# Performance work log

Hardware: AMD Instinct MI355X
Metric: run time of the kernel (lower is better)

The kernel has to match this reference:

```python
import math
import jax, jax.numpy as jnp
import numpy as np

H, DK = 16, 64            # n_heads, d_kv
NUM_BUCKETS, MAX_DIST = 32, 128


def _relative_position_buckets(S):
    # Bidirectional (encoder) T5 bucketization of relative positions.
    ctx = jnp.arange(S, dtype=jnp.int32)[:, None]      # query positions
    mem = jnp.arange(S, dtype=jnp.int32)[None, :]      # key positions
    rp = mem - ctx                                     # [S, S]
    nb = NUM_BUCKETS // 2
    rb = (rp > 0).astype(jnp.int32) * nb
    n = jnp.abs(rp)
    max_exact = nb // 2
    is_small = n < max_exact
    large = max_exact + (
        jnp.log(jnp.maximum(n, 1).astype(jnp.float32) / max_exact)
        / math.log(MAX_DIST / max_exact)
        * (nb - max_exact)
    ).astype(jnp.int32)
    large = jnp.minimum(large, nb - 1)
    return rb + jnp.where(is_small, n, large)          # [S, S] int32


def setup_inputs() -> dict:
    key = jax.random.key(0)
    ks = jax.random.split(key, 6)
    B, S, D = 4, 1024, 1024
    inner = H * DK
    std = 0.02
    return {
        "hidden_states": jax.random.normal(ks[0], (B, S, D), jnp.float32),
        "Wq": jax.random.normal(ks[1], (inner, D), jnp.float32) * std,
        "Wk": jax.random.normal(ks[2], (inner, D), jnp.float32) * std,
        "Wv": jax.random.normal(ks[3], (inner, D), jnp.float32) * std,
        "Wo": jax.random.normal(ks[4], (D, inner), jnp.float32) * std,
        "rel_bias": jax.random.normal(ks[5], (NUM_BUCKETS, H), jnp.float32) * std,
    }


def reference(hidden_states, Wq, Wk, Wv, Wo, rel_bias):
    B, S, D = hidden_states.shape

    def proj(W):  # bias-free linear + split heads -> [B, H, S, DK]
        return (hidden_states @ W.T).reshape(B, S, H, DK).transpose(0, 2, 1, 3)

    q, k, v = proj(Wq), proj(Wk), proj(Wv)
    # T5: NO 1/sqrt(d) scaling
    scores = jnp.einsum("bhqd,bhkd->bhqk", q, k)       # [B, H, S, S]
    bias = rel_bias[_relative_position_buckets(S)]     # [S, S, H]
    scores = scores + bias.transpose(2, 0, 1)[None]    # broadcast over batch
    attn = jax.nn.softmax(scores, axis=-1)
    ctx = jnp.einsum("bhqk,bhkd->bhqd", attn, v)       # [B, H, S, DK]
    ctx = ctx.transpose(0, 2, 1, 3).reshape(B, S, H * DK)
    return ctx @ Wo.T                                  # [B, S, D]
```

## Files before the change

### kernel.cpp

```cpp
#include <hip/hip_runtime.h>

typedef _Float16 half8 __attribute__((ext_vector_type(8)));
typedef _Float16 half4_t __attribute__((ext_vector_type(4)));
typedef float f32x4 __attribute__((ext_vector_type(4)));

#define GK 1024
#define MEG (1024 * 1024)
#define LOG2E 1.44269504088896f

#define GLD16(gptr, lptr) \
    __builtin_amdgcn_global_load_lds((const __attribute__((address_space(1))) void*)(gptr), \
                                     (__attribute__((address_space(3))) void*)(lptr), 16, 0, 0)

__global__ void cvt_all_kernel(const float* __restrict__ hidden,
                               const float* __restrict__ Wq,
                               const float* __restrict__ Wk,
                               const float* __restrict__ Wv,
                               const float* __restrict__ Wo,
                               _Float16* __restrict__ ws) {
    int b = blockIdx.x;
    const float* src;
    _Float16* dst;
    if (b < 4096)      { src = hidden; dst = ws; }
    else if (b < 5120) { src = Wq; dst = ws + 4 * MEG; b -= 4096; }
    else if (b < 6144) { src = Wk; dst = ws + 5 * MEG; b -= 5120; }
    else if (b < 7168) { src = Wv; dst = ws + 6 * MEG; b -= 6144; }
    else               { src = Wo; dst = ws + 7 * MEG; b -= 7168; }
    int i = (b * 256 + threadIdx.x) * 4;
    f32x4 v = *(const f32x4*)(src + i);
    half4_t h;
    h[0] = (_Float16)v[0]; h[1] = (_Float16)v[1];
    h[2] = (_Float16)v[2]; h[3] = (_Float16)v[3];
    *(half4_t*)(dst + i) = h;
}

__global__ __launch_bounds__(256) void gemm_qkv_kernel(
    const _Float16* __restrict__ A,
    const _Float16* __restrict__ B0,
    const _Float16* __restrict__ B1,
    const _Float16* __restrict__ B2,
    _Float16* __restrict__ O0,
    _Float16* __restrict__ O1,
    _Float16* __restrict__ O2)
{
    const int lid = blockIdx.x;
    const int xcd = lid & 7;
    const int rr = lid >> 3;
    const int xb = rr & 7;
    const int gg = xcd * 12 + (rr >> 3);
    const int yb = gg & 31;
    const int z  = gg >> 5;
    const _Float16* Bw = (z == 0) ? B0 : ((z == 1) ? B1 : B2);
    _Float16* Oh = (z == 0) ? O0 : ((z == 1) ? O1 : O2);

    __shared__ __attribute__((aligned(16))) _Float16 sA[2][128][32];
    __shared__ __attribute__((aligned(16))) _Float16 sB[2][128][32];

    const int tid = threadIdx.x;
    const int wave = tid >> 6, lane = tid & 63;
    const int quad = lane >> 4, l16 = lane & 15;
    const int wr = wave >> 1, wc = wave & 1;
    const int M0 = yb * 128, N0 = xb * 128;

    const int rl = lane >> 2;
    const int cl = (lane & 3) * 8;
    const size_t aRow0 = (size_t)(M0 + wave * 16 + rl) * GK + cl;
    const size_t aRow1 = aRow0 + (size_t)64 * GK;
    const size_t bRow0 = (size_t)(N0 + wave * 16 + rl) * GK + cl;
    const size_t bRow1 = bRow0 + (size_t)64 * GK;
    _Float16* ldsA[2][2] = {{&sA[0][wave * 16][0], &sA[0][64 + wave * 16][0]},
                            {&sA[1][wave * 16][0], &sA[1][64 + wave * 16][0]}};
    _Float16* ldsB[2][2] = {{&sB[0][wave * 16][0], &sB[0][64 + wave * 16][0]},
                            {&sB[1][wave * 16][0], &sB[1][64 + wave * 16][0]}};

    f32x4 acc[4][4] = {};

    for (int kt = 0; kt < GK / 64; ++kt) {
        const int ko = kt * 64;
        #pragma unroll
        for (int c = 0; c < 2; ++c) {
            GLD16(A + aRow0 + ko + c * 32, ldsA[c][0]);
            GLD16(A + aRow1 + ko + c * 32, ldsA[c][1]);
            GLD16(Bw + bRow0 + ko + c * 32, ldsB[c][0]);
            GLD16(Bw + bRow1 + ko + c * 32, ldsB[c][1]);
        }
        __syncthreads();
        #pragma unroll
        for (int c = 0; c < 2; ++c) {
            half8 af[4], bf[4];
            #pragma unroll
            for (int i = 0; i < 4; ++i)
                af[i] = *(const half8*)&sA[c][wr * 64 + i * 16 + l16][quad * 8];
            #pragma unroll
            for (int j = 0; j < 4; ++j)
                bf[j] = *(const half8*)&sB[c][wc * 64 + j * 16 + l16][quad * 8];
            #pragma unroll
            for (int i = 0; i < 4; ++i)
                #pragma unroll
                for (int j = 0; j < 4; ++j)
                    acc[i][j] = __builtin_amdgcn_mfma_f32_16x16x32_f16(af[i], bf[j], acc[i][j], 0, 0, 0);
        }
        __syncthreads();
    }

    if (z == 2) {
        #pragma unroll
        for (int i = 0; i < 4; ++i) {
            #pragma unroll
            for (int j = 0; j < 4; ++j) {
                int m = M0 + wr * 64 + i * 16 + quad * 4;
                int n = N0 + wc * 64 + j * 16 + l16;
                int b = m >> 10, s = m & 1023, hh = n >> 6, d = n & 63;
                half4_t o;
                #pragma unroll
                for (int r = 0; r < 4; ++r) o[r] = (_Float16)acc[i][j][r];
                *(half4_t*)&Oh[((size_t)((b * 16 + hh) * 64 + d)) * 1024 + s] = o;
            }
        }
    } else {
        #pragma unroll
        for (int i = 0; i < 4; ++i) {
            #pragma unroll
            for (int j = 0; j < 4; ++j) {
                #pragma unroll
                for (int r = 0; r < 4; ++r) {
                    int m = M0 + wr * 64 + i * 16 + quad * 4 + r;
                    int n = N0 + wc * 64 + j * 16 + l16;
                    int b = m >> 10, s = m & 1023, hh = n >> 6, d = n & 63;
                    Oh[((size_t)((b * 16 + hh) * 1024 + s)) * 64 + d] = (_Float16)acc[i][j][r];
                }
            }
        }
    }
}

__global__ __launch_bounds__(256) void gemm_o_kernel(
    const _Float16* __restrict__ A,
    const _Float16* __restrict__ Bw,
    float* __restrict__ Of)
{
    const int lid = blockIdx.x;
    const int xcd = lid & 7;
    const int rr = lid >> 3;
    const int xb = rr & 7;
    const int yb = xcd * 8 + (rr >> 3);

    __shared__ __attribute__((aligned(16))) _Float16 sA[2][64][32];
    __shared__ __attribute__((aligned(16))) _Float16 sB[2][128][32];

    const int tid = threadIdx.x;
    const int wave = tid >> 6, lane = tid & 63;
    const int quad = lane >> 4, l16 = lane & 15;
    const int M0 = yb * 64, N0 = xb * 128;

    const int rl = lane >> 2;
    const int cl = (lane & 3) * 8;
    const size_t aRow  = (size_t)(M0 + wave * 16 + rl) * GK + cl;
    const size_t bRow0 = (size_t)(N0 + wave * 16 + rl) * GK + cl;
    const size_t bRow1 = bRow0 + (size_t)64 * GK;
    _Float16* ldsA[2]    = {&sA[0][wave * 16][0], &sA[1][wave * 16][0]};
    _Float16* ldsB[2][2] = {{&sB[0][wave * 16][0], &sB[0][64 + wave * 16][0]},
                            {&sB[1][wave * 16][0], &sB[1][64 + wave * 16][0]}};

    f32x4 acc[4][2] = {};

    for (int kt = 0; kt < GK / 64; ++kt) {
        const int ko = kt * 64;
        #pragma unroll
        for (int c = 0; c < 2; ++c) {
            GLD16(A + aRow + ko + c * 32, ldsA[c]);
            GLD16(Bw + bRow0 + ko + c * 32, ldsB[c][0]);
            GLD16(Bw + bRow1 + ko + c * 32, ldsB[c][1]);
        }
        __syncthreads();
        #pragma unroll
        for (int c = 0; c < 2; ++c) {
            half8 af[4], bf[2];
            #pragma unroll
            for (int i = 0; i < 4; ++i)
                af[i] = *(const half8*)&sA[c][i * 16 + l16][quad * 8];
            #pragma unroll
            for (int j = 0; j < 2; ++j)
                bf[j] = *(const half8*)&sB[c][wave * 32 + j * 16 + l16][quad * 8];
            #pragma unroll
            for (int i = 0; i < 4; ++i)
                #pragma unroll
                for (int j = 0; j < 2; ++j)
                    acc[i][j] = __builtin_amdgcn_mfma_f32_16x16x32_f16(af[i], bf[j], acc[i][j], 0, 0, 0);
        }
        __syncthreads();
    }

    #pragma unroll
    for (int i = 0; i < 4; ++i) {
        #pragma unroll
        for (int j = 0; j < 2; ++j) {
            #pragma unroll
            for (int r = 0; r < 4; ++r) {
                int m = M0 + i * 16 + quad * 4 + r;
                int n = N0 + wave * 32 + j * 16 + l16;
                Of[(size_t)m * 1024 + n] = acc[i][j][r];
            }
        }
    }
}

__global__ __launch_bounds__(256) void attn_kernel(
    const _Float16* __restrict__ Q,
    const _Float16* __restrict__ K,
    const _Float16* __restrict__ VT,
    const float* __restrict__ rel_bias,
    _Float16* __restrict__ ctx)
{
    const int S = 1024;
    const int qt = blockIdx.x;
    const int q0 = qt * 64;
    const int h = blockIdx.y;
    const int b = blockIdx.z;
    const int bh = b * 16 + h;
    const _Float16* Qh = Q + (size_t)bh * S * 64;
    const _Float16* Kh = K + (size_t)bh * S * 64;
    const _Float16* VTh = VT + (size_t)bh * 64 * S;

    __shared__ __attribute__((aligned(16))) _Float16 sQ[64][72];
    __shared__ __attribute__((aligned(16))) _Float16 sK[64][72];
    __shared__ __attribute__((aligned(16))) _Float16 sVt[64][72];
    __shared__ __attribute__((aligned(16))) _Float16 sP[4][16][72];
    __shared__ _Float16 sBias[1088];

    const int tid = threadIdx.x;
    const int wave = tid >> 6, lane = tid & 63;
    const int quad = lane >> 4, l16 = lane & 15;

    {
        int r = tid >> 3, c = (tid & 7) * 8;
        *(half8*)&sQ[r][c]      = *(const half8*)(Qh + (size_t)(q0 + r) * 64 + c);
        *(half8*)&sQ[r + 32][c] = *(const half8*)(Qh + (size_t)(q0 + r + 32) * 64 + c);
    }
    for (int i = tid; i < 1087; i += 256) {
        int delta = i - (q0 + 63);
        int rb = (delta > 0) ? 16 : 0;
        int n = (delta < 0) ? -delta : delta;
        int bucket;
        if (n < 8) bucket = rb + n;
        else bucket = rb + 8 + (n >= 12) + (n >= 16) + (n >= 23) + (n >= 32)
                             + (n >= 46) + (n >= 64) + (n >= 91);
        sBias[i] = (_Float16)rel_bias[bucket * 16 + h];
    }
    __syncthreads();

    half8 qf0 = *(const half8*)&sQ[wave * 16 + l16][quad * 8];
    half8 qf1 = *(const half8*)&sQ[wave * 16 + l16][32 + quad * 8];

    const int sr = tid >> 3;
    const int sc_ = (tid & 7) * 8;
    const _Float16* kp0 = Kh + (size_t)sr * 64 + sc_;
    const _Float16* kp1 = kp0 + (size_t)32 * 64;
    const _Float16* vp0 = VTh + (size_t)sr * S + sc_;
    const _Float16* vp1 = vp0 + (size_t)32 * S;
    _Float16* sKw0 = &sK[sr][sc_];
    _Float16* sKw1 = &sK[sr + 32][sc_];
    _Float16* sVw0 = &sVt[sr][sc_];
    _Float16* sVw1 = &sVt[sr + 32][sc_];

    half8 rk0 = *(const half8*)kp0;
    half8 rk1 = *(const half8*)kp1;
    half8 rv0 = *(const half8*)vp0;
    half8 rv1 = *(const half8*)vp1;
    kp0 += 4096; kp1 += 4096; vp0 += 64; vp1 += 64;

    float m_run = -INFINITY, l_run = 0.0f;
    f32x4 acc[4] = {};

    for (int kt = 0; kt < 16; ++kt) {
        __syncthreads();
        *(half8*)sKw0 = rk0;
        *(half8*)sKw1 = rk1;
        *(half8*)sVw0 = rv0;
        *(half8*)sVw1 = rv1;
        __syncthreads();
        if (kt < 15) {
            rk0 = *(const half8*)kp0;
            rk1 = *(const half8*)kp1;
            rv0 = *(const half8*)vp0;
            rv1 = *(const half8*)vp1;
            kp0 += 4096; kp1 += 4096; vp0 += 64; vp1 += 64;
        }

        f32x4 sc[4] = {};
        #pragma unroll
        for (int j = 0; j < 4; ++j) {
            half8 kf0 = *(const half8*)&sK[j * 16 + l16][quad * 8];
            half8 kf1 = *(const half8*)&sK[j * 16 + l16][32 + quad * 8];
            sc[j] = __builtin_amdgcn_mfma_f32_16x16x32_f16(kf0, qf0, sc[j], 0, 0, 0);
            sc[j] = __builtin_amdgcn_mfma_f32_16x16x32_f16(kf1, qf1, sc[j], 0, 0, 0);
        }

        const int bbase = kt * 64 + quad * 4 - wave * 16 - l16 + 63;
        float ps = 0.0f;
        if (kt <= qt - 3 || kt >= qt + 3) {
            const float cb = (float)sBias[bbase];
            float mx = fmaxf(fmaxf(fmaxf(sc[0][0], sc[0][1]), fmaxf(sc[0][2], sc[0][3])),
                             fmaxf(fmaxf(sc[1][0], sc[1][1]), fmaxf(sc[1][2], sc[1][3])));
            mx = fmaxf(mx, fmaxf(fmaxf(fmaxf(sc[2][0], sc[2][1]), fmaxf(sc[2][2], sc[2][3])),
                                 fmaxf(fmaxf(sc[3][0], sc[3][1]), fmaxf(sc[3][2], sc[3][3]))));
            mx = fmaxf(mx, __shfl_xor(mx, 16));
            mx = fmaxf(mx, __shfl_xor(mx, 32));
            float mnew = fmaxf(m_run, mx + cb);
            float alpha = __expf(m_run - mnew);
            m_run = mnew;
            const float kk = (cb - mnew) * LOG2E;
            #pragma unroll
            for (int j = 0; j < 4; ++j) {
                half4_t pw;
                #pragma unroll
                for (int r = 0; r < 4; ++r) {
                    float p = __builtin_exp2f(__builtin_fmaf(sc[j][r], LOG2E, kk));
                    ps += p;
                    pw[r] = (_Float16)p;
                }
                *(half4_t*)&sP[wave][l16][j * 16 + quad * 4] = pw;
            }
            l_run = l_run * alpha + ps;
            #pragma unroll
            for (int dt = 0; dt < 4; ++dt) acc[dt] *= alpha;
        } else {
            #pragma unroll
            for (int j = 0; j < 4; ++j)
                #pragma unroll
                for (int r = 0; r < 4; ++r)
                    sc[j][r] += (float)sBias[bbase + j * 16 + r];
            float mx = fmaxf(fmaxf(fmaxf(sc[0][0], sc[0][1]), fmaxf(sc[0][2], sc[0][3])),
                             fmaxf(fmaxf(sc[1][0], sc[1][1]), fmaxf(sc[1][2], sc[1][3])));
            mx = fmaxf(mx, fmaxf(fmaxf(fmaxf(sc[2][0], sc[2][1]), fmaxf(sc[2][2], sc[2][3])),
                                 fmaxf(fmaxf(sc[3][0], sc[3][1]), fmaxf(sc[3][2], sc[3][3]))));
            mx = fmaxf(mx, __shfl_xor(mx, 16));
            mx = fmaxf(mx, __shfl_xor(mx, 32));
            float mnew = fmaxf(m_run, mx);
            float alpha = __expf(m_run - mnew);
            m_run = mnew;
            #pragma unroll
            for (int j = 0; j < 4; ++j) {
                half4_t pw;
                #pragma unroll
                for (int r = 0; r < 4; ++r) {
                    float p = __expf(sc[j][r] - mnew);
                    ps += p;
                    pw[r] = (_Float16)p;
                }
                *(half4_t*)&sP[wave][l16][j * 16 + quad * 4] = pw;
            }
            l_run = l_run * alpha + ps;
            #pragma unroll
            for (int dt = 0; dt < 4; ++dt) acc[dt] *= alpha;
        }

        half8 pf0 = *(const half8*)&sP[wave][l16][quad * 8];
        half8 pf1 = *(const half8*)&sP[wave][l16][32 + quad * 8];
        #pragma unroll
        for (int dt = 0; dt < 4; ++dt) {
            half8 vf0 = *(const half8*)&sVt[dt * 16 + l16][quad * 8];
            half8 vf1 = *(const half8*)&sVt[dt * 16 + l16][32 + quad * 8];
            acc[dt] = __builtin_amdgcn_mfma_f32_16x16x32_f16(vf0, pf0, acc[dt], 0, 0, 0);
            acc[dt] = __builtin_amdgcn_mfma_f32_16x16x32_f16(vf1, pf1, acc[dt], 0, 0, 0);
        }
    }

    l_run += __shfl_xor(l_run, 16);
    l_run += __shfl_xor(l_run, 32);
    const float inv = 1.0f / l_run;
    const size_t qg = (size_t)(b * 1024 + q0 + wave * 16 + l16);
    #pragma unroll
    for (int dt = 0; dt < 4; ++dt) {
        half4_t o;
        #pragma unroll
        for (int r = 0; r < 4; ++r) o[r] = (_Float16)(acc[dt][r] * inv);
        *(half4_t*)&ctx[qg * 1024 + h * 64 + dt * 16 + quad * 4] = o;
    }
}

extern "C" void kernel_launch(void* const* d_in, const int* in_sizes, int n_in,
                              void* d_out, int out_size, void* d_ws, size_t ws_size,
                              hipStream_t stream) {
    const float* hidden   = (const float*)d_in[0];
    const float* Wq       = (const float*)d_in[1];
    const float* Wk       = (const float*)d_in[2];
    const float* Wv       = (const float*)d_in[3];
    const float* Wo       = (const float*)d_in[4];
    const float* rel_bias = (const float*)d_in[5];
    float* out = (float*)d_out;

    _Float16* ws    = (_Float16*)d_ws;
    _Float16* h16   = ws;
    _Float16* wq16  = ws + 4 * (size_t)MEG;
    _Float16* wk16  = ws + 5 * (size_t)MEG;
    _Float16* wv16  = ws + 6 * (size_t)MEG;
    _Float16* wo16  = ws + 7 * (size_t)MEG;
    _Float16* Qs    = ws + 8 * (size_t)MEG;
    _Float16* Ks    = ws + 12 * (size_t)MEG;
    _Float16* VTs   = ws + 16 * (size_t)MEG;
    _Float16* ctx16 = ws + 20 * (size_t)MEG;

    cvt_all_kernel<<<8192, 256, 0, stream>>>(hidden, Wq, Wk, Wv, Wo, ws);

    gemm_qkv_kernel<<<dim3(768), 256, 0, stream>>>(
        h16, wq16, wk16, wv16, Qs, Ks, VTs);

    attn_kernel<<<dim3(16, 16, 4), 256, 0, stream>>>(Qs, Ks, VTs, rel_bias, ctx16);

    gemm_o_kernel<<<dim3(512), 256, 0, stream>>>(ctx16, wo16, out);
}
```

Measured before the change: 191.6 us.

## Enlarge attention tiles to 128x128 with 512 threads and remap QKV GEMM blocks

The attention kernel now processes 128 queries per block with 8 waves and steps through keys in 128-wide tiles, so each block loads K and V half as many times. The two softmax branches are merged into one path with a uniform-bias flag, and P·V is done in two 64-key halves that reuse the same per-wave P buffer. The QKV GEMM block index mapping is changed so each XCD handles four fixed row blocks across all three weights, aiming for better L2 reuse of the activation matrix. The costs are fewer blocks in the attention launch and higher register and LDS use per block, which could reduce occupancy.

Measured after the change: 200.3 us. +4.5%, slower.

```diff
diff --git a/kernel.cpp b/kernel.cpp
--- a/kernel.cpp
+++ b/kernel.cpp
@@ -47,9 +47,9 @@
     const int xcd = lid & 7;
     const int rr = lid >> 3;
     const int xb = rr & 7;
-    const int gg = xcd * 12 + (rr >> 3);
-    const int yb = gg & 31;
-    const int z  = gg >> 5;
+    const int gidx = rr >> 3;
+    const int yb = xcd * 4 + (gidx & 3);
+    const int z  = gidx >> 2;
     const _Float16* Bw = (z == 0) ? B0 : ((z == 1) ? B1 : B2);
     _Float16* Oh = (z == 0) ? O0 : ((z == 1) ? O1 : O2);
 
@@ -205,7 +205,7 @@
     }
 }
 
-__global__ __launch_bounds__(256) void attn_kernel(
+__global__ __launch_bounds__(512) void attn_kernel(
     const _Float16* __restrict__ Q,
     const _Float16* __restrict__ K,
     const _Float16* __restrict__ VT,
@@ -214,7 +214,7 @@
 {
     const int S = 1024;
     const int qt = blockIdx.x;
-    const int q0 = qt * 64;
+    const int q0 = qt * 128;
     const int h = blockIdx.y;
     const int b = blockIdx.z;
     const int bh = b * 16 + h;
@@ -222,11 +222,11 @@
     const _Float16* Kh = K + (size_t)bh * S * 64;
     const _Float16* VTh = VT + (size_t)bh * 64 * S;
 
-    __shared__ __attribute__((aligned(16))) _Float16 sQ[64][72];
-    __shared__ __attribute__((aligned(16))) _Float16 sK[64][72];
-    __shared__ __attribute__((aligned(16))) _Float16 sVt[64][72];
-    __shared__ __attribute__((aligned(16))) _Float16 sP[4][16][72];
-    __shared__ _Float16 sBias[1088];
+    __shared__ __attribute__((aligned(16))) _Float16 sQ[128][72];
+    __shared__ __attribute__((aligned(16))) _Float16 sK[128][72];
+    __shared__ __attribute__((aligned(16))) _Float16 sVt[64][136];
+    __shared__ __attribute__((aligned(16))) _Float16 sP[8][16][72];
+    __shared__ _Float16 sBias[1152];
 
     const int tid = threadIdx.x;
     const int wave = tid >> 6, lane = tid & 63;
@@ -235,10 +235,10 @@
     {
         int r = tid >> 3, c = (tid & 7) * 8;
         *(half8*)&sQ[r][c]      = *(const half8*)(Qh + (size_t)(q0 + r) * 64 + c);
-        *(half8*)&sQ[r + 32][c] = *(const half8*)(Qh + (size_t)(q0 + r + 32) * 64 + c);
-    }
-    for (int i = tid; i < 1087; i += 256) {
-        int delta = i - (q0 + 63);
+        *(half8*)&sQ[r + 64][c] = *(const half8*)(Qh + (size_t)(q0 + r + 64) * 64 + c);
+    }
+    for (int i = tid; i < 1151; i += 512) {
+        int delta = i - (q0 + 127);
         int rb = (delta > 0) ? 16 : 0;
         int n = (delta < 0) ? -delta : delta;
         int bucket;
@@ -255,115 +255,126 @@
     const int sr = tid >> 3;
     const int sc_ = (tid & 7) * 8;
     const _Float16* kp0 = Kh + (size_t)sr * 64 + sc_;
-    const _Float16* kp1 = kp0 + (size_t)32 * 64;
-    const _Float16* vp0 = VTh + (size_t)sr * S + sc_;
+    const _Float16* kp1 = kp0 + (size_t)64 * 64;
+    _Float16* sKw0 = &sK[sr][sc_];
+    _Float16* sKw1 = &sK[sr + 64][sc_];
+    const int vr = tid >> 4;
+    const int vc = (tid & 15) * 8;
+    const _Float16* vp0 = VTh + (size_t)vr * S + vc;
     const _Float16* vp1 = vp0 + (size_t)32 * S;
-    _Float16* sKw0 = &sK[sr][sc_];
-    _Float16* sKw1 = &sK[sr + 32][sc_];
-    _Float16* sVw0 = &sVt[sr][sc_];
-    _Float16* sVw1 = &sVt[sr + 32][sc_];
+    _Float16* sVw0 = &sVt[vr][vc];
+    _Float16* sVw1 = &sVt[vr + 32][vc];
 
     half8 rk0 = *(const half8*)kp0;
     half8 rk1 = *(const half8*)kp1;
     half8 rv0 = *(const half8*)vp0;
     half8 rv1 = *(const half8*)vp1;
-    kp0 += 4096; kp1 += 4096; vp0 += 64; vp1 += 64;
+    kp0 += 8192; kp1 += 8192; vp0 += 128; vp1 += 128;
 
     float m_run = -INFINITY, l_run = 0.0f;
     f32x4 acc[4] = {};
 
-    for (int kt = 0; kt < 16; ++kt) {
+    for (int kt = 0; kt < 8; ++kt) {
         __syncthreads();
         *(half8*)sKw0 = rk0;
         *(half8*)sKw1 = rk1;
         *(half8*)sVw0 = rv0;
         *(half8*)sVw1 = rv1;
         __syncthreads();
-        if (kt < 15) {
+        if (kt < 7) {
             rk0 = *(const half8*)kp0;
             rk1 = *(const half8*)kp1;
             rv0 = *(const half8*)vp0;
             rv1 = *(const half8*)vp1;
-            kp0 += 4096; kp1 += 4096; vp0 += 64; vp1 += 64;
-        }
-
-        f32x4 sc[4] = {};
-        #pragma unroll
-        for (int j = 0; j < 4; ++j) {
+            kp0 += 8192; kp1 += 8192; vp0 += 128; vp1 += 128;
+        }
+
+        f32x4 sc[8] = {};
+        #pragma unroll
+        for (int j = 0; j < 8; ++j) {
             half8 kf0 = *(const half8*)&sK[j * 16 + l16][quad * 8];
             half8 kf1 = *(const half8*)&sK[j * 16 + l16][32 + quad * 8];
             sc[j] = __builtin_amdgcn_mfma_f32_16x16x32_f16(kf0, qf0, sc[j], 0, 0, 0);
             sc[j] = __builtin_amdgcn_mfma_f32_16x16x32_f16(kf1, qf1, sc[j], 0, 0, 0);
         }
 
-        const int bbase = kt * 64 + quad * 4 - wave * 16 - l16 + 63;
-        float ps = 0.0f;
-        if (kt <= qt - 3 || kt >= qt + 3) {
-            const float cb = (float)sBias[bbase];
-            float mx = fmaxf(fmaxf(fmaxf(sc[0][0], sc[0][1]), fmaxf(sc[0][2], sc[0][3])),
-                             fmaxf(fmaxf(sc[1][0], sc[1][1]), fmaxf(sc[1][2], sc[1][3])));
-            mx = fmaxf(mx, fmaxf(fmaxf(fmaxf(sc[2][0], sc[2][1]), fmaxf(sc[2][2], sc[2][3])),
-                                 fmaxf(fmaxf(sc[3][0], sc[3][1]), fmaxf(sc[3][2], sc[3][3]))));
-            mx = fmaxf(mx, __shfl_xor(mx, 16));
-            mx = fmaxf(mx, __shfl_xor(mx, 32));
-            float mnew = fmaxf(m_run, mx + cb);
-            float alpha = __expf(m_run - mnew);
-            m_run = mnew;
-            const float kk = (cb - mnew) * LOG2E;
-            #pragma unroll
-            for (int j = 0; j < 4; ++j) {
-                half4_t pw;
-                #pragma unroll
-                for (int r = 0; r < 4; ++r) {
-                    float p = __builtin_exp2f(__builtin_fmaf(sc[j][r], LOG2E, kk));
-                    ps += p;
-                    pw[r] = (_Float16)p;
-                }
-                *(half4_t*)&sP[wave][l16][j * 16 + quad * 4] = pw;
-            }
-            l_run = l_run * alpha + ps;
-            #pragma unroll
-            for (int dt = 0; dt < 4; ++dt) acc[dt] *= alpha;
+        const int bbase = kt * 128 + quad * 4 - wave * 16 - l16 + 127;
+        const bool uni = (kt <= qt - 2) || (kt >= qt + 2);
+        float cb = 0.0f;
+        if (uni) {
+            cb = (float)sBias[bbase];
         } else {
             #pragma unroll
-            for (int j = 0; j < 4; ++j)
+            for (int j = 0; j < 8; ++j)
                 #pragma unroll
                 for (int r = 0; r < 4; ++r)
                     sc[j][r] += (float)sBias[bbase + j * 16 + r];
-            float mx = fmaxf(fmaxf(fmaxf(sc[0][0], sc[0][1]), fmaxf(sc[0][2], sc[0][3])),
-                             fmaxf(fmaxf(sc[1][0], sc[1][1]), fmaxf(sc[1][2], sc[1][3])));
-            mx = fmaxf(mx, fmaxf(fmaxf(fmaxf(sc[2][0], sc[2][1]), fmaxf(sc[2][2], sc[2][3])),
-                                 fmaxf(fmaxf(sc[3][0], sc[3][1]), fmaxf(sc[3][2], sc[3][3]))));
-            mx = fmaxf(mx, __shfl_xor(mx, 16));
-            mx = fmaxf(mx, __shfl_xor(mx, 32));
-            float mnew = fmaxf(m_run, mx);
-            float alpha = __expf(m_run - mnew);
-            m_run = mnew;
-            #pragma unroll
-            for (int j = 0; j < 4; ++j) {
-                half4_t pw;
-                #pragma unroll
-                for (int r = 0; r < 4; ++r) {
-                    float p = __expf(sc[j][r] - mnew);
-                    ps += p;
-                    pw[r] = (_Float16)p;
-                }
-                *(half4_t*)&sP[wave][l16][j * 16 + quad * 4] = pw;
-            }
-            l_run = l_run * alpha + ps;
-            #pragma unroll
-            for (int dt = 0; dt < 4; ++dt) acc[dt] *= alpha;
-        }
-
-        half8 pf0 = *(const half8*)&sP[wave][l16][quad * 8];
-        half8 pf1 = *(const half8*)&sP[wave][l16][32 + quad * 8];
-        #pragma unroll
-        for (int dt = 0; dt < 4; ++dt) {
-            half8 vf0 = *(const half8*)&sVt[dt * 16 + l16][quad * 8];
-            half8 vf1 = *(const half8*)&sVt[dt * 16 + l16][32 + quad * 8];
-            acc[dt] = __builtin_amdgcn_mfma_f32_16x16x32_f16(vf0, pf0, acc[dt], 0, 0, 0);
-            acc[dt] = __builtin_amdgcn_mfma_f32_16x16x32_f16(vf1, pf1, acc[dt], 0, 0, 0);
-        }
+        }
+        float t0 = fmaxf(fmaxf(sc[0][0], sc[0][1]), fmaxf(sc[0][2], sc[0][3]));
+        float t1 = fmaxf(fmaxf(sc[1][0], sc[1][1]), fmaxf(sc[1][2], sc[1][3]));
+        float t2 = fmaxf(fmaxf(sc[2][0], sc[2][1]), fmaxf(sc[2][2], sc[2][3]));
+        float t3 = fmaxf(fmaxf(sc[3][0], sc[3][1]), fmaxf(sc[3][2], sc[3][3]));
+        float t4 = fmaxf(fmaxf(sc[4][0], sc[4][1]), fmaxf(sc[4][2], sc[4][3]));
+        float t5 = fmaxf(fmaxf(sc[5][0], sc[5][1]), fmaxf(sc[5][2], sc[5][3]));
+        float t6 = fmaxf(fmaxf(sc[6][0], sc[6][1]), fmaxf(sc[6][2], sc[6][3]));
+        float t7 = fmaxf(fmaxf(sc[7][0], sc[7][1]), fmaxf(sc[7][2], sc[7][3]));
+        float mx = fmaxf(fmaxf(fmaxf(t0, t1), fmaxf(t2, t3)),
+                         fmaxf(fmaxf(t4, t5), fmaxf(t6, t7)));
+        mx = fmaxf(mx, __shfl_xor(mx, 16));
+        mx = fmaxf(mx, __shfl_xor(mx, 32));
+        float mnew = fmaxf(m_run, uni ? mx + cb : mx);
+        float alpha = __expf(m_run - mnew);
+        m_run = mnew;
+        const float kk = ((uni ? cb : 0.0f) - mnew) * LOG2E;
+        #pragma unroll
+        for (int dt = 0; dt < 4; ++dt) acc[dt] *= alpha;
+        float ps = 0.0f;
+
+        #pragma unroll
+        for (int j = 0; j < 4; ++j) {
+            half4_t pw;
+            #pragma unroll
+            for (int r = 0; r < 4; ++r) {
+                float p = __builtin_exp2f(__builtin_fmaf(sc[j][r], LOG2E, kk));
+                ps += p;
+                pw[r] = (_Float16)p;
+            }
+            *(half4_t*)&sP[wave][l16][j * 16 + quad * 4] = pw;
+        }
+        {
+            half8 pf0 = *(const half8*)&sP[wave][l16][quad * 8];
+            half8 pf1 = *(const half8*)&sP[wave][l16][32 + quad * 8];
+            #pragma unroll
+            for (int dt = 0; dt < 4; ++dt) {
+                half8 vf0 = *(const half8*)&sVt[dt * 16 + l16][quad * 8];
+                half8 vf1 = *(const half8*)&sVt[dt * 16 + l16][32 + quad * 8];
+                acc[dt] = __builtin_amdgcn_mfma_f32_16x16x32_f16(vf0, pf0, acc[dt], 0, 0, 0);
+                acc[dt] = __builtin_amdgcn_mfma_f32_16x16x32_f16(vf1, pf1, acc[dt], 0, 0, 0);
+            }
+        }
+        #pragma unroll
+        for (int j = 4; j < 8; ++j) {
+            half4_t pw;
+            #pragma unroll
+            for (int r = 0; r < 4; ++r) {
+                float p = __builtin_exp2f(__builtin_fmaf(sc[j][r], LOG2E, kk));
+                ps += p;
+                pw[r] = (_Float16)p;
+            }
+            *(half4_t*)&sP[wave][l16][(j - 4) * 16 + quad * 4] = pw;
+        }
+        {
+            half8 pf0 = *(const half8*)&sP[wave][l16][quad * 8];
+            half8 pf1 = *(const half8*)&sP[wave][l16][32 + quad * 8];
+            #pragma unroll
+            for (int dt = 0; dt < 4; ++dt) {
+                half8 vf0 = *(const half8*)&sVt[dt * 16 + l16][64 + quad * 8];
+                half8 vf1 = *(const half8*)&sVt[dt * 16 + l16][96 + quad * 8];
+                acc[dt] = __builtin_amdgcn_mfma_f32_16x16x32_f16(vf0, pf0, acc[dt], 0, 0, 0);
+                acc[dt] = __builtin_amdgcn_mfma_f32_16x16x32_f16(vf1, pf1, acc[dt], 0, 0, 0);
+            }
+        }
+        l_run = l_run * alpha + ps;
     }
 
     l_run += __shfl_xor(l_run, 16);
@@ -406,7 +417,7 @@
     gemm_qkv_kernel<<<dim3(768), 256, 0, stream>>>(
         h16, wq16, wk16, wv16, Qs, Ks, VTs);
 
-    attn_kernel<<<dim3(16, 16, 4), 256, 0, stream>>>(Qs, Ks, VTs, rel_bias, ctx16);
+    attn_kernel<<<dim3(8, 16, 4), 512, 0, stream>>>(Qs, Ks, VTs, rel_bias, ctx16);
 
     gemm_o_kernel<<<dim3(512), 256, 0, stream>>>(ctx16, wo16, out);
 }
```
